# Optimization experiments

Measured on AMD Instinct MI355X. Metric: run time of the kernel, lower is better.

The kernel has to match this reference:

```python
import jax, jax.numpy as jnp
import numpy as np

D_MODEL = 768
NHEAD = 12
HEAD_DIM = D_MODEL // NHEAD
WINDOW = 33  # band half-width = 16


def setup_inputs() -> dict:
    key = jax.random.key(0)
    ks = jax.random.split(key, 9)
    B, T, C = 2, 4096, D_MODEL
    s = 0.02
    return {
        "x": jax.random.normal(ks[0], (B, T, C), jnp.float32),
        "Wq": jax.random.normal(ks[1], (C, C), jnp.float32) * s,
        "bq": jnp.zeros((C,), jnp.float32),
        "Wk": jax.random.normal(ks[2], (C, C), jnp.float32) * s,
        "bk": jnp.zeros((C,), jnp.float32),
        "Wv": jax.random.normal(ks[3], (C, C), jnp.float32) * s,
        "bv": jnp.zeros((C,), jnp.float32),
        "Wo": jax.random.normal(ks[4], (C, C), jnp.float32) * s,
        "bo": jnp.zeros((C,), jnp.float32),
    }


def reference(x, Wq, bq, Wk, bk, Wv, bv, Wo, bo):
    B, T, C = x.shape
    H, D = NHEAD, HEAD_DIM
    scale = D ** -0.5
    # torch Linear: x @ W.T + b
    q = (x @ Wq.T + bq).reshape(B, T, H, D).transpose(0, 2, 1, 3)  # [B,H,T,D]
    k = (x @ Wk.T + bk).reshape(B, T, H, D).transpose(0, 2, 1, 3)
    v = (x @ Wv.T + bv).reshape(B, T, H, D).transpose(0, 2, 1, 3)
    scores = jnp.einsum("bhqd,bhkd->bhqk", q, k) * scale  # [B,H,T,T]
    idx = jnp.arange(T)
    local_mask = jnp.abs(idx[:, None] - idx[None, :]) <= (WINDOW // 2)  # [T,T]
    scores = jnp.where(local_mask[None, None], scores, -jnp.inf)
    attn = jax.nn.softmax(scores, axis=-1)  # dropout=0 / eval mode
    out = jnp.einsum("bhqk,bhkd->bhqd", attn, v)  # [B,H,T,D]
    out = out.transpose(0, 2, 1, 3).reshape(B, T, C)
    return out @ Wo.T + bo
```

## Files before the change

kernel.cpp:

```cpp
#include <hip/hip_runtime.h>
#include <math.h>
#include <cstdint>
#include <cstddef>

typedef unsigned short u16;
typedef short bf16x8 __attribute__((ext_vector_type(8)));
typedef float f32x4 __attribute__((ext_vector_type(4)));
typedef u16 u16x8 __attribute__((ext_vector_type(8)));
typedef u16 u16x4 __attribute__((ext_vector_type(4)));

#define T_LEN 4096
#define NH 12
#define HD 64
#define DMODEL 768
#define GK 768
#define QKV_STRIDE 6291456ul

__device__ __forceinline__ u16 f2bf(float x) {
  union { float f; unsigned u; } v; v.f = x;
  unsigned r = v.u + 0x7fffu + ((v.u >> 16) & 1u);
  return (u16)(r >> 16);
}
__device__ __forceinline__ float bf2f(u16 x) {
  union { unsigned u; float f; } v; v.u = ((unsigned)x) << 16;
  return v.f;
}
__device__ __forceinline__ void bfpair(unsigned u, float& lo, float& hi) {
  union { unsigned u; float f; } a, b;
  a.u = u << 16; b.u = u & 0xffff0000u;
  lo = a.f; hi = b.f;
}

__device__ __forceinline__ void async16(const u16* g, u16* l) {
  __builtin_amdgcn_global_load_lds(
      (const __attribute__((address_space(1))) unsigned int*)g,
      (__attribute__((address_space(3))) unsigned int*)l, 16, 0, 0);
}

__global__ void cvt_f32_bf16(const float* __restrict__ s, u16* __restrict__ d, int n) {
  int i = (blockIdx.x * blockDim.x + threadIdx.x) * 4;
  if (i >= n) return;
  float4 v = *(const float4*)(s + i);
  u16x4 o;
  o[0] = f2bf(v.x); o[1] = f2bf(v.y); o[2] = f2bf(v.z); o[3] = f2bf(v.w);
  *(u16x4*)(d + i) = o;
}

__global__ void cvt_w4(const float* __restrict__ s0, const float* __restrict__ s1,
                       const float* __restrict__ s2, const float* __restrict__ s3,
                       u16* __restrict__ d0, u16* __restrict__ d1,
                       u16* __restrict__ d2, u16* __restrict__ d3) {
  const float* s; u16* d;
  switch (blockIdx.y) {
    case 0: s = s0; d = d0; break;
    case 1: s = s1; d = d1; break;
    case 2: s = s2; d = d2; break;
    default: s = s3; d = d3; break;
  }
  int i = (blockIdx.x * blockDim.x + threadIdx.x) * 4;
  float4 v = *(const float4*)(s + i);
  u16x4 o;
  o[0] = f2bf(v.x); o[1] = f2bf(v.y); o[2] = f2bf(v.z); o[3] = f2bf(v.w);
  *(u16x4*)(d + i) = o;
}

#define BM 128
#define BN 128
#define BK 32

template <int EPI>
__global__ __launch_bounds__(256)
void gemm_bt(const u16* __restrict__ A, const u16* __restrict__ B,
             const float* __restrict__ bias0, const float* __restrict__ bias1,
             const float* __restrict__ bias2, void* __restrict__ outp) {
  __shared__ __align__(16) u16 As[BM * BK];
  __shared__ __align__(16) u16 Bs[BN * BK];
  const int tid  = threadIdx.x;
  const int lane = tid & 63;
  const int wave = tid >> 6;
  const int wm = wave & 1, wn = wave >> 1;
  const long am0 = (long)blockIdx.x * BM;
  const long bn0 = (long)blockIdx.y * BN;
  const int r16 = lane & 15;
  const int kh  = lane >> 4;

  f32x4 acc[4][4] = {};

  const int srow = lane >> 2;
  const int skc  = (lane & 3) * 8;
  const u16* Ag = A + (am0 + wave * 16 + srow) * GK + skc;
  const u16* Bg = B + (bn0 + wave * 16 + srow) * GK + skc;
  u16* Al0 = &As[(wave * 16) * BK];
  u16* Al1 = &As[(64 + wave * 16) * BK];
  u16* Bl0 = &Bs[(wave * 16) * BK];
  u16* Bl1 = &Bs[(64 + wave * 16) * BK];

  for (int kt = 0; kt < GK; kt += BK) {
    __syncthreads();
    async16(Ag + kt, Al0);
    async16(Ag + 64 * GK + kt, Al1);
    async16(Bg + kt, Bl0);
    async16(Bg + 64 * GK + kt, Bl1);
    __syncthreads();
    bf16x8 af[4], bfr[4];
#pragma unroll
    for (int i = 0; i < 4; i++)
      af[i] = *(const bf16x8*)&As[(wm * 64 + i * 16 + r16) * BK + kh * 8];
#pragma unroll
    for (int j = 0; j < 4; j++)
      bfr[j] = *(const bf16x8*)&Bs[(wn * 64 + j * 16 + r16) * BK + kh * 8];
#pragma unroll
    for (int i = 0; i < 4; i++)
#pragma unroll
      for (int j = 0; j < 4; j++)
        acc[i][j] = __builtin_amdgcn_mfma_f32_16x16x32_bf16(af[i], bfr[j], acc[i][j], 0, 0, 0);
  }

  const int m0 = (int)am0 + wm * 64;
  const int n0 = (int)bn0 + wn * 64;
  if (EPI == 0) {
    u16* qkv = (u16*)outp;
#pragma unroll
    for (int j = 0; j < 4; j++) {
      int col = n0 + j * 16 + r16;
      int tens = col / 768;
      int c = col - tens * 768;
      const float* bp = (tens == 0) ? bias0 : ((tens == 1) ? bias1 : bias2);
      float bv = bp[c];
      int hh = c >> 6, dd = c & 63;
#pragma unroll
      for (int i = 0; i < 4; i++) {
#pragma unroll
        for (int r = 0; r < 4; r++) {
          int row = m0 + i * 16 + kh * 4 + r;
          int b_ = row >> 12, t = row & 4095;
          size_t off = (size_t)tens * QKV_STRIDE +
                       ((((size_t)(b_ * NH + hh)) * T_LEN + t) << 6) + dd;
          qkv[off] = f2bf(acc[i][j][r] + bv);
        }
      }
    }
  } else {
    float* O = (float*)outp;
#pragma unroll
    for (int i = 0; i < 4; i++) {
#pragma unroll
      for (int r = 0; r < 4; r++) {
        int row = m0 + i * 16 + kh * 4 + r;
        float* orow = O + (size_t)row * DMODEL;
#pragma unroll
        for (int j = 0; j < 4; j++) {
          int col = n0 + j * 16 + r16;
          orow[col] = acc[i][j][r] + bias0[col];
        }
      }
    }
  }
}

#define QB 64
#define SLAB 96
#define KSTR 72

__global__ __launch_bounds__(256)
void attn_local(const u16* __restrict__ qkv, u16* __restrict__ attn) {
  __shared__ __align__(16) u16 Ks[SLAB][KSTR];
  __shared__ __align__(16) u16 Vs[SLAB][KSTR];
  const int tid = threadIdx.x;
  const int q0 = blockIdx.x * QB;
  const int h = blockIdx.y, b = blockIdx.z;
  const size_t head = ((size_t)(b * NH + h)) * (T_LEN * HD);
  const u16* Qg = qkv + head;
  const u16* Kg = qkv + QKV_STRIDE + head;
  const u16* Vg = qkv + 2 * QKV_STRIDE + head;

  for (int e = tid; e < SLAB * 8; e += 256) {
    int r = e >> 3, c8 = (e & 7) * 8;
    int g = q0 - 16 + r;
    if (g >= 0 && g < T_LEN) {
      *(u16x8*)&Ks[r][c8] = *(const u16x8*)(Kg + (size_t)g * HD + c8);
      *(u16x8*)&Vs[r][c8] = *(const u16x8*)(Vg + (size_t)g * HD + c8);
    } else {
      u16x8 zz = {0, 0, 0, 0, 0, 0, 0, 0};
      *(u16x8*)&Ks[r][c8] = zz;
      *(u16x8*)&Vs[r][c8] = zz;
    }
  }

  const int qi = tid >> 2;
  const int p  = tid & 3;
  const int d0 = p * 16;
  const int t  = q0 + qi;

  float qv[16];
  {
    uint4 a = *(const uint4*)(Qg + (size_t)t * HD + d0);
    uint4 bq = *(const uint4*)(Qg + (size_t)t * HD + d0 + 8);
    bfpair(a.x, qv[0], qv[1]);   bfpair(a.y, qv[2], qv[3]);
    bfpair(a.z, qv[4], qv[5]);   bfpair(a.w, qv[6], qv[7]);
    bfpair(bq.x, qv[8], qv[9]);  bfpair(bq.y, qv[10], qv[11]);
    bfpair(bq.z, qv[12], qv[13]); bfpair(bq.w, qv[14], qv[15]);
  }
  __syncthreads();

  float s[33];
#pragma unroll
  for (int j = 0; j < 33; j++) {
    const int row = qi + j;
    uint4 a = *(const uint4*)&Ks[row][d0];
    uint4 c = *(const uint4*)&Ks[row][d0 + 8];
    float k0, k1;
    float a0 = 0.f, a1 = 0.f;
    bfpair(a.x, k0, k1); a0 += qv[0] * k0;  a1 += qv[1] * k1;
    bfpair(a.y, k0, k1); a0 += qv[2] * k0;  a1 += qv[3] * k1;
    bfpair(a.z, k0, k1); a0 += qv[4] * k0;  a1 += qv[5] * k1;
    bfpair(a.w, k0, k1); a0 += qv[6] * k0;  a1 += qv[7] * k1;
    bfpair(c.x, k0, k1); a0 += qv[8] * k0;  a1 += qv[9] * k1;
    bfpair(c.y, k0, k1); a0 += qv[10] * k0; a1 += qv[11] * k1;
    bfpair(c.z, k0, k1); a0 += qv[12] * k0; a1 += qv[13] * k1;
    bfpair(c.w, k0, k1); a0 += qv[14] * k0; a1 += qv[15] * k1;
    float sc = a0 + a1;
    sc += __shfl_xor(sc, 1);
    sc += __shfl_xor(sc, 2);
    int kidx = t - 16 + j;
    s[j] = (kidx >= 0 && kidx < T_LEN) ? sc * 0.125f : -INFINITY;
  }

  float m = s[0];
#pragma unroll
  for (int j = 1; j < 33; j++) m = fmaxf(m, s[j]);
  float l = 0.f;
#pragma unroll
  for (int j = 0; j < 33; j++) {
    float pp = __expf(s[j] - m);
    s[j] = pp;
    l += pp;
  }
  float inv = 1.0f / l;

  float o[16] = {};
#pragma unroll
  for (int j = 0; j < 33; j++) {
    const int row = qi + j;
    float pp = s[j];
    uint4 a = *(const uint4*)&Vs[row][d0];
    uint4 c = *(const uint4*)&Vs[row][d0 + 8];
    float v0, v1;
    bfpair(a.x, v0, v1); o[0]  += pp * v0; o[1]  += pp * v1;
    bfpair(a.y, v0, v1); o[2]  += pp * v0; o[3]  += pp * v1;
    bfpair(a.z, v0, v1); o[4]  += pp * v0; o[5]  += pp * v1;
    bfpair(a.w, v0, v1); o[6]  += pp * v0; o[7]  += pp * v1;
    bfpair(c.x, v0, v1); o[8]  += pp * v0; o[9]  += pp * v1;
    bfpair(c.y, v0, v1); o[10] += pp * v0; o[11] += pp * v1;
    bfpair(c.z, v0, v1); o[12] += pp * v0; o[13] += pp * v1;
    bfpair(c.w, v0, v1); o[14] += pp * v0; o[15] += pp * v1;
  }

  u16* orow = attn + ((size_t)(b * T_LEN + t)) * DMODEL + h * HD + d0;
  u16x8 ov;
#pragma unroll
  for (int z = 0; z < 8; z++) ov[z] = f2bf(o[z] * inv);
  *(u16x8*)orow = ov;
#pragma unroll
  for (int z = 0; z < 8; z++) ov[z] = f2bf(o[8 + z] * inv);
  *(u16x8*)(orow + 8) = ov;
}

extern "C" void kernel_launch(void* const* d_in, const int* in_sizes, int n_in,
                              void* d_out, int out_size, void* d_ws, size_t ws_size,
                              hipStream_t stream) {
  const float* x  = (const float*)d_in[0];
  const float* Wq = (const float*)d_in[1];
  const float* bq = (const float*)d_in[2];
  const float* Wk = (const float*)d_in[3];
  const float* bk = (const float*)d_in[4];
  const float* Wv = (const float*)d_in[5];
  const float* bv = (const float*)d_in[6];
  const float* Wo = (const float*)d_in[7];
  const float* bo = (const float*)d_in[8];
  float* out = (float*)d_out;
  char* ws = (char*)d_ws;

  u16* xb   = (u16*)(ws);
  u16* wqkv = (u16*)(ws + 12582912);
  u16* wo_b = (u16*)(ws + 16121856);
  u16* qkv  = (u16*)(ws + 17301504);
  u16* attn = (u16*)(ws + 55050240);

  cvt_f32_bf16<<<6144, 256, 0, stream>>>(x, xb, 6291456);
  cvt_w4<<<dim3(576, 4), 256, 0, stream>>>(Wq, Wk, Wv, Wo,
                                           wqkv, wqkv + 589824, wqkv + 1179648, wo_b);

  gemm_bt<0><<<dim3(64, 18), 256, 0, stream>>>(xb, wqkv, bq, bk, bv, (void*)qkv);
  attn_local<<<dim3(64, 12, 2), 256, 0, stream>>>(qkv, attn);
  gemm_bt<1><<<dim3(64, 6), 256, 0, stream>>>(attn, wo_b, bo, bo, bo, (void*)out);
}
```

Baseline: 189.2 us.

## Store QKV token-major via LDS-staged epilogue and swizzle GEMM shared tiles

The QKV GEMM epilogue now stages each bf16 output tile in shared memory and writes 16-byte coalesced rows into a [B,T,768] layout. Before, each thread did scattered 2-byte stores into a head-major [B,H,T,D] layout. The attention kernel is changed to read Q/K/V and index its output with the new row stride. The GEMM shared-memory tiles also get an XOR chunk swizzle to cut LDS bank conflicts, and shared memory becomes dynamic, which raises the QKV GEMM's LDS use and may lower occupancy.

```diff
diff --git a/kernel.cpp b/kernel.cpp
--- a/kernel.cpp
+++ b/kernel.cpp
@@ -73,8 +73,11 @@
 void gemm_bt(const u16* __restrict__ A, const u16* __restrict__ B,
              const float* __restrict__ bias0, const float* __restrict__ bias1,
              const float* __restrict__ bias2, void* __restrict__ outp) {
-  __shared__ __align__(16) u16 As[BM * BK];
-  __shared__ __align__(16) u16 Bs[BN * BK];
+  extern __shared__ __align__(16) u16 smem[];
+  u16* As = smem;
+  u16* Bs = smem + BM * BK;
+  u16* Cs = smem + (BM + BN) * BK;
+
   const int tid  = threadIdx.x;
   const int lane = tid & 63;
   const int wave = tid >> 6;
@@ -83,13 +86,14 @@
   const long bn0 = (long)blockIdx.y * BN;
   const int r16 = lane & 15;
   const int kh  = lane >> 4;
+  const int sw8 = (kh ^ ((r16 >> 1) & 3)) * 8;
 
   f32x4 acc[4][4] = {};
 
-  const int srow = lane >> 2;
-  const int skc  = (lane & 3) * 8;
-  const u16* Ag = A + (am0 + wave * 16 + srow) * GK + skc;
-  const u16* Bg = B + (bn0 + wave * 16 + srow) * GK + skc;
+  const int srow   = lane >> 2;
+  const int schunk = ((lane & 3) ^ ((lane >> 3) & 3)) * 8;
+  const u16* Ag = A + (am0 + wave * 16 + srow) * GK + schunk;
+  const u16* Bg = B + (bn0 + wave * 16 + srow) * GK + schunk;
   u16* Al0 = &As[(wave * 16) * BK];
   u16* Al1 = &As[(64 + wave * 16) * BK];
   u16* Bl0 = &Bs[(wave * 16) * BK];
@@ -105,10 +109,10 @@
     bf16x8 af[4], bfr[4];
 #pragma unroll
     for (int i = 0; i < 4; i++)
-      af[i] = *(const bf16x8*)&As[(wm * 64 + i * 16 + r16) * BK + kh * 8];
+      af[i] = *(const bf16x8*)&As[(wm * 64 + i * 16 + r16) * BK + sw8];
 #pragma unroll
     for (int j = 0; j < 4; j++)
-      bfr[j] = *(const bf16x8*)&Bs[(wn * 64 + j * 16 + r16) * BK + kh * 8];
+      bfr[j] = *(const bf16x8*)&Bs[(wn * 64 + j * 16 + r16) * BK + sw8];
 #pragma unroll
     for (int i = 0; i < 4; i++)
 #pragma unroll
@@ -117,28 +121,33 @@
   }
 
   const int m0 = (int)am0 + wm * 64;
-  const int n0 = (int)bn0 + wn * 64;
+  const int n0w = wn * 64;
+
   if (EPI == 0) {
-    u16* qkv = (u16*)outp;
+    const int tens = (int)(bn0 >= 1536 ? 2 : (bn0 >= 768 ? 1 : 0));
+    const int c0 = (int)bn0 - tens * 768;
+    const float* bp = (tens == 0) ? bias0 : ((tens == 1) ? bias1 : bias2);
+    u16* outb = (u16*)outp + (size_t)tens * QKV_STRIDE;
+
 #pragma unroll
     for (int j = 0; j < 4; j++) {
-      int col = n0 + j * 16 + r16;
-      int tens = col / 768;
-      int c = col - tens * 768;
-      const float* bp = (tens == 0) ? bias0 : ((tens == 1) ? bias1 : bias2);
-      float bv = bp[c];
-      int hh = c >> 6, dd = c & 63;
+      float bv = bp[c0 + n0w + j * 16 + r16];
+      int lc = n0w + j * 16 + r16;
 #pragma unroll
       for (int i = 0; i < 4; i++) {
-#pragma unroll
-        for (int r = 0; r < 4; r++) {
-          int row = m0 + i * 16 + kh * 4 + r;
-          int b_ = row >> 12, t = row & 4095;
-          size_t off = (size_t)tens * QKV_STRIDE +
-                       ((((size_t)(b_ * NH + hh)) * T_LEN + t) << 6) + dd;
-          qkv[off] = f2bf(acc[i][j][r] + bv);
-        }
+        int lr = wm * 64 + i * 16 + kh * 4;
+#pragma unroll
+        for (int r = 0; r < 4; r++)
+          Cs[(lr + r) * BN + lc] = f2bf(acc[i][j][r] + bv);
       }
+    }
+    __syncthreads();
+#pragma unroll
+    for (int z = 0; z < 8; z++) {
+      int cidx = z * 256 + tid;
+      int row = cidx >> 4, ch = (cidx & 15) * 8;
+      uint4 val = *(const uint4*)&Cs[row * BN + ch];
+      *(uint4*)(outb + (size_t)(am0 + row) * DMODEL + c0 + ch) = val;
     }
   } else {
     float* O = (float*)outp;
@@ -150,7 +159,7 @@
         float* orow = O + (size_t)row * DMODEL;
 #pragma unroll
         for (int j = 0; j < 4; j++) {
-          int col = n0 + j * 16 + r16;
+          int col = (int)bn0 + n0w + j * 16 + r16;
           orow[col] = acc[i][j][r] + bias0[col];
         }
       }
@@ -169,17 +178,19 @@
   const int tid = threadIdx.x;
   const int q0 = blockIdx.x * QB;
   const int h = blockIdx.y, b = blockIdx.z;
-  const size_t head = ((size_t)(b * NH + h)) * (T_LEN * HD);
-  const u16* Qg = qkv + head;
-  const u16* Kg = qkv + QKV_STRIDE + head;
-  const u16* Vg = qkv + 2 * QKV_STRIDE + head;
+  const size_t rowbase = (size_t)b * T_LEN;
+  const int hc = h * HD;
+  const u16* Qg = qkv;
+  const u16* Kg = qkv + QKV_STRIDE;
+  const u16* Vg = qkv + 2 * QKV_STRIDE;
 
   for (int e = tid; e < SLAB * 8; e += 256) {
     int r = e >> 3, c8 = (e & 7) * 8;
     int g = q0 - 16 + r;
     if (g >= 0 && g < T_LEN) {
-      *(u16x8*)&Ks[r][c8] = *(const u16x8*)(Kg + (size_t)g * HD + c8);
-      *(u16x8*)&Vs[r][c8] = *(const u16x8*)(Vg + (size_t)g * HD + c8);
+      size_t off = (rowbase + g) * DMODEL + hc + c8;
+      *(u16x8*)&Ks[r][c8] = *(const u16x8*)(Kg + off);
+      *(u16x8*)&Vs[r][c8] = *(const u16x8*)(Vg + off);
     } else {
       u16x8 zz = {0, 0, 0, 0, 0, 0, 0, 0};
       *(u16x8*)&Ks[r][c8] = zz;
@@ -194,8 +205,9 @@
 
   float qv[16];
   {
-    uint4 a = *(const uint4*)(Qg + (size_t)t * HD + d0);
-    uint4 bq = *(const uint4*)(Qg + (size_t)t * HD + d0 + 8);
+    const u16* qrow = Qg + (rowbase + t) * DMODEL + hc + d0;
+    uint4 a = *(const uint4*)qrow;
+    uint4 bq = *(const uint4*)(qrow + 8);
     bfpair(a.x, qv[0], qv[1]);   bfpair(a.y, qv[2], qv[3]);
     bfpair(a.z, qv[4], qv[5]);   bfpair(a.w, qv[6], qv[7]);
     bfpair(bq.x, qv[8], qv[9]);  bfpair(bq.y, qv[10], qv[11]);
@@ -256,7 +268,7 @@
     bfpair(c.w, v0, v1); o[14] += pp * v0; o[15] += pp * v1;
   }
 
-  u16* orow = attn + ((size_t)(b * T_LEN + t)) * DMODEL + h * HD + d0;
+  u16* orow = attn + (rowbase + t) * DMODEL + hc + d0;
   u16x8 ov;
 #pragma unroll
   for (int z = 0; z < 8; z++) ov[z] = f2bf(o[z] * inv);
@@ -291,7 +303,7 @@
   cvt_w4<<<dim3(576, 4), 256, 0, stream>>>(Wq, Wk, Wv, Wo,
                                            wqkv, wqkv + 589824, wqkv + 1179648, wo_b);
 
-  gemm_bt<0><<<dim3(64, 18), 256, 0, stream>>>(xb, wqkv, bq, bk, bv, (void*)qkv);
+  gemm_bt<0><<<dim3(64, 18), 256, 49152, stream>>>(xb, wqkv, bq, bk, bv, (void*)qkv);
   attn_local<<<dim3(64, 12, 2), 256, 0, stream>>>(qkv, attn);
-  gemm_bt<1><<<dim3(64, 6), 256, 0, stream>>>(attn, wo_b, bo, bo, bo, (void*)out);
-}
+  gemm_bt<1><<<dim3(64, 6), 256, 16384, stream>>>(attn, wo_b, bo, bo, bo, (void*)out);
+}
```

New measurement: 187.6 us. Within noise of the previous version (-0.9%).
